# Optimization experiments

Hardware: AMD Instinct MI355X
Metric: run time of the kernel (lower is better)

The kernel has to match this reference:

```python
import jax, jax.numpy as jnp
import numpy as np

B, S, R, Z, NLHS = 1024, 277, 76, 56, 24  # batch, seq_len, n_rules, z_size, n_lhs_symbols


def setup_inputs() -> dict:
    key = jax.random.key(0)
    k1, k2, k3, k4, k5, k6 = jax.random.split(key, 6)
    model_out_x = jax.random.normal(k1, (B, S, R), jnp.float32)
    mu = jax.random.normal(k2, (B, Z), jnp.float32)
    log_var = 0.1 * jax.random.normal(k3, (B, Z), jnp.float32)
    # one-hot targets over rules
    tgt_idx = jax.random.randint(k4, (B, S), 0, R)
    target_x = jax.nn.one_hot(tgt_idx, R, dtype=jnp.float32)
    # binary allowed-transition masks per LHS symbol
    masks = (jax.random.uniform(k5, (NLHS, R)) < 0.3).astype(jnp.float32)
    masks = masks.at[:, 0].set(1.0)  # ensure no all-zero mask row
    ind_to_lhs_ind = jax.random.randint(k6, (R,), 0, NLHS)
    return dict(model_out_x=model_out_x, mu=mu, log_var=log_var,
                target_x=target_x, masks=masks, ind_to_lhs_ind=ind_to_lhs_ind)


def reference(model_out_x, mu, log_var, target_x, masks, ind_to_lhs_ind):
    b = model_out_x.shape[0]
    seq_len = model_out_x.shape[1]
    z_size = mu.shape[1]

    # --- apply_masks: vectorized gather replacing the nested python loops ---
    true_rule = jnp.argmax(target_x, axis=-1)          # [B,S]
    lhs = ind_to_lhs_ind[true_rule]                    # [B,S]
    mask = masks[lhs]                                  # [B,S,R]
    shift_to_tiny = -100.0 + (model_out_x.min() - model_out_x.max())
    x = model_out_x + (1.0 - mask) * shift_to_tiny

    # --- softmax + BCE (torch BCELoss clamps log terms at -100) ---
    p = jax.nn.softmax(x, axis=-1)
    log_p = jnp.maximum(jnp.log(p), -100.0)
    log_1mp = jnp.maximum(jnp.log1p(-p), -100.0)
    bce = -jnp.mean(target_x * log_p + (1.0 - target_x) * log_1mp)
    BCE = seq_len * bce

    # --- moment-matching error on mu ---
    avg_mu = jnp.sum(mu, axis=0) / b                   # [Z]
    var = (mu.T @ mu) / b                              # [Z,Z]
    var_err = var - jnp.eye(z_size, dtype=mu.dtype)
    var_err = jnp.tanh(var_err) * var_err
    mom_err = jnp.sum(avg_mu * avg_mu) / z_size + jnp.sum(var_err) / (z_size * z_size)

    # sample_z=False, module in training mode -> loss = BCE + mom_err
    return BCE + mom_err
```

## Files before the change

### kernel.cpp

```cpp
#include <hip/hip_runtime.h>
#include <math.h>

#define BB    1024
#define SS    277
#define RR    76
#define ZZ    56
#define NLHS  24
#define NROWS (BB*SS)
#define ROWS_PER_BLOCK 256
#define NBCE (NROWS/ROWS_PER_BLOCK)
#define NMOM ZZ
#define NBLK (NBCE + NMOM)
#define F4ROW 19
#define F4BLK (ROWS_PER_BLOCK*F4ROW)
#define BLK_ELEMS (ROWS_PER_BLOCK*RR)
#define TOTAL_ELEMS 21558272.0

static_assert(NROWS % ROWS_PER_BLOCK == 0, "rows divide blocks");

#define LN2F  0.69314718056f
#define NLN2F (-144.26950409f)

__device__ __forceinline__ void gload_lds16(const float4* g, float4* l) {
    auto gp = reinterpret_cast<const __attribute__((address_space(1))) unsigned int*>(
        reinterpret_cast<uintptr_t>(g));
    auto lp = reinterpret_cast<__attribute__((address_space(3))) unsigned int*>(
        reinterpret_cast<uintptr_t>(l));
    __builtin_amdgcn_global_load_lds(gp, lp, 16, 0, 0);
}

__global__ __launch_bounds__(256, 2) void fused_kernel(
    const float* __restrict__ model,
    const float* __restrict__ target,
    const float* __restrict__ masks,
    const int*   __restrict__ ind_to_lhs,
    const float* __restrict__ mu,
    double* __restrict__ partials)
{
    __shared__ float4        sx[F4BLK];
    __shared__ unsigned int  smb[NLHS*4];
    __shared__ int           sm_lhs[RR];
    __shared__ unsigned char sm_idx[ROWS_PER_BLOCK];
    __shared__ float         sm_red[4];
    __shared__ float         sdot[4][64];
    __shared__ float         ssum[4];

    const int tid = threadIdx.x;

    if (blockIdx.x < NMOM) {
        const int j    = blockIdx.x;
        const int w    = tid >> 6;
        const int lane = tid & 63;
        const int i    = (lane < ZZ) ? lane : 0;
        float dot = 0.f, s1 = 0.f;
        const int b0 = 256*w;
        #pragma unroll 4
        for (int b = b0; b < b0 + 256; ++b) {
            const float c = mu[b*ZZ + j];
            const float a = mu[b*ZZ + i];
            dot = fmaf(a, c, dot);
            s1 += c;
        }
        sdot[w][lane] = dot;
        if (lane == 0) ssum[w] = s1;
        __syncthreads();
        if (w == 0) {
            float term = 0.f;
            if (lane < ZZ) {
                const float var = (sdot[0][lane]+sdot[1][lane]+sdot[2][lane]+sdot[3][lane]) * (1.f/BB);
                const float ve  = var - ((lane == j) ? 1.f : 0.f);
                term = tanhf(ve) * ve * (1.f/(ZZ*ZZ));
                if (lane == j) {
                    const float am = (ssum[0]+ssum[1]+ssum[2]+ssum[3]) * (1.f/BB);
                    term = fmaf(am*am, 1.f/ZZ, term);
                }
            }
            #pragma unroll
            for (int off = 32; off; off >>= 1) term += __shfl_xor(term, off, 64);
            if (lane == 0) partials[blockIdx.x] = (double)term;
        }
        return;
    }

    const int bce_blk = blockIdx.x - NMOM;
    const size_t blk_base = (size_t)bce_blk * BLK_ELEMS;

    if (tid < NLHS*4) smb[tid] = 0u;
    sm_idx[tid] = 0;
    __syncthreads();

    float4 t[F4ROW];
    {
        const float4* t4 = (const float4*)(target + blk_base);
        #pragma unroll
        for (int k = 0; k < F4ROW; ++k) t[k] = t4[tid + 256*k];
    }
    {
        const float4* g4 = (const float4*)(model + blk_base);
        #pragma unroll
        for (int k = 0; k < F4ROW; ++k)
            gload_lds16(g4 + tid + 256*k, &sx[tid + 256*k]);
    }

    for (int e = tid; e < NLHS*RR; e += 256) {
        const int lhs = e / RR;
        const int r   = e - lhs*RR;
        if (masks[e] > 0.5f)
            atomicOr(&smb[lhs*4 + (r >> 5)], 1u << (r & 31));
    }
    if (tid < RR) sm_lhs[tid] = ind_to_lhs[tid];

    #pragma unroll
    for (int k = 0; k < F4ROW; ++k) {
        const int v4 = tid + 256*k;
        const float4 tv = t[k];
        int he = -1;
        const int e = v4*4;
        if (tv.x > 0.5f) he = e;
        if (tv.y > 0.5f) he = e+1;
        if (tv.z > 0.5f) he = e+2;
        if (tv.w > 0.5f) he = e+3;
        if (he >= 0) {
            const int row = he / RR;
            sm_idx[row] = (unsigned char)(he - row*RR);
        }
    }
    __syncthreads();

    const int true_r = (int)sm_idx[tid];
    const int lhs    = sm_lhs[true_r];
    const unsigned int mw0 = smb[lhs*4 + 0];
    const unsigned int mw1 = smb[lhs*4 + 1];
    const unsigned int mw2 = smb[lhs*4 + 2];

    const float4* xr = &sx[tid*F4ROW];

    float mx = -1e30f;
    #pragma unroll
    for (int k = 0; k < F4ROW; ++k) {
        const float4 v = xr[k];
        #pragma unroll
        for (int c = 0; c < 4; ++c) {
            const int r = k*4 + c;
            const unsigned int mw = (r < 32) ? mw0 : ((r < 64) ? mw1 : mw2);
            const bool un = (mw >> (r & 31)) & 1u;
            const float xm = un ? (&v.x)[c] : -1e30f;
            mx = fmaxf(mx, xm);
        }
    }

    float s = 0.f;
    #pragma unroll
    for (int k = 0; k < F4ROW; ++k) {
        const float4 v = xr[k];
        #pragma unroll
        for (int c = 0; c < 4; ++c) {
            const int r = k*4 + c;
            const unsigned int mw = (r < 32) ? mw0 : ((r < 64) ? mw1 : mw2);
            const bool un = (mw >> (r & 31)) & 1u;
            const float xm = un ? (&v.x)[c] : -1e30f;
            s += __expf(xm - mx);
        }
    }

    const float inv = 1.f / s;
    float sum_l2 = 0.f;
    float p_true = 0.f;
    #pragma unroll
    for (int k = 0; k < F4ROW; ++k) {
        const float4 v = xr[k];
        #pragma unroll
        for (int c = 0; c < 4; ++c) {
            const int r = k*4 + c;
            const unsigned int mw = (r < 32) ? mw0 : ((r < 64) ? mw1 : mw2);
            const bool un = (mw >> (r & 31)) & 1u;
            const float xm = un ? (&v.x)[c] : -1e30f;
            const float ev = __expf(xm - mx);
            const float p  = ev * inv;
            const float l2 = __log2f(1.f - p);
            sum_l2 += fmaxf(l2, NLN2F);
            if (r == true_r) p_true = p;
        }
    }
    float row_sum = LN2F * sum_l2;
    const float l1c_t = fmaxf(LN2F * __log2f(1.f - p_true), -100.f);
    const float lp_t  = fmaxf(__logf(p_true), -100.f);
    row_sum += lp_t - l1c_t;

    #pragma unroll
    for (int off = 32; off; off >>= 1) row_sum += __shfl_xor(row_sum, off, 64);
    if ((tid & 63) == 0) sm_red[tid >> 6] = row_sum;
    __syncthreads();
    if (tid == 0)
        partials[blockIdx.x] = (double)((sm_red[0] + sm_red[1]) + (sm_red[2] + sm_red[3]));
}

__global__ __launch_bounds__(256) void final_kernel(
    const double* __restrict__ partials, float* __restrict__ out)
{
    __shared__ double sred[4];
    const int tid = threadIdx.x;
    double s = 0.0;
    for (int k = NMOM + tid; k < NBLK; k += 256) s += partials[k];
    double m = (tid < NMOM) ? partials[tid] : 0.0;
    double val = s * (-(double)SS / TOTAL_ELEMS) + m;
    #pragma unroll
    for (int off = 32; off; off >>= 1) val += __shfl_xor(val, off, 64);
    if ((tid & 63) == 0) sred[tid >> 6] = val;
    __syncthreads();
    if (tid == 0) out[0] = (float)((sred[0] + sred[1]) + (sred[2] + sred[3]));
}

extern "C" void kernel_launch(void* const* d_in, const int* in_sizes, int n_in,
                              void* d_out, int out_size, void* d_ws, size_t ws_size,
                              hipStream_t stream) {
    const float* model  = (const float*)d_in[0];
    const float* mu     = (const float*)d_in[1];
    const float* target = (const float*)d_in[3];
    const float* masks  = (const float*)d_in[4];
    const int*   ind    = (const int*)  d_in[5];
    float* out  = (float*)d_out;
    double* acc = (double*)d_ws;

    fused_kernel<<<NBLK, ROWS_PER_BLOCK, 0, stream>>>(model, target, masks, ind, mu, acc);
    final_kernel<<<1, 256, 0, stream>>>(acc, out);
}
```

Baseline: 215.4 us.

## Convert BCE blocks to persistent loop with double-buffered LDS prefetch

The BCE part of the kernel now launches a fixed 256 blocks instead of one block per 256-row group. Each block loops over groups with a stride of 256. While it computes the current group, it fetches the next group's target one-hot indices and issues global-to-LDS loads of the model logits into a second LDS buffer. The goal is to hide global memory latency behind the softmax/BCE math and to cut per-block launch and setup cost. In exchange, LDS use doubles to about 155KB per block, so each CU holds one block of 4 waves instead of two. With 1108 groups the work also ends unevenly: some blocks run 5 iterations and others 4.

```diff
diff --git a/kernel.cpp b/kernel.cpp
--- a/kernel.cpp
+++ b/kernel.cpp
@@ -11,12 +11,13 @@
 #define NBCE (NROWS/ROWS_PER_BLOCK)
 #define NMOM ZZ
 #define NBLK (NBCE + NMOM)
+#define PBLK 256
 #define F4ROW 19
 #define F4BLK (ROWS_PER_BLOCK*F4ROW)
 #define BLK_ELEMS (ROWS_PER_BLOCK*RR)
 #define TOTAL_ELEMS 21558272.0
 
-static_assert(NROWS % ROWS_PER_BLOCK == 0, "rows divide blocks");
+static_assert(NROWS % ROWS_PER_BLOCK == 0, "rows divide groups");
 
 #define LN2F  0.69314718056f
 #define NLN2F (-144.26950409f)
@@ -29,7 +30,7 @@
     __builtin_amdgcn_global_load_lds(gp, lp, 16, 0, 0);
 }
 
-__global__ __launch_bounds__(256, 2) void fused_kernel(
+__global__ __launch_bounds__(256, 1) void fused_kernel(
     const float* __restrict__ model,
     const float* __restrict__ target,
     const float* __restrict__ masks,
@@ -37,11 +38,11 @@
     const float* __restrict__ mu,
     double* __restrict__ partials)
 {
-    __shared__ float4        sx[F4BLK];
+    __shared__ float4        sx[2][F4BLK];
     __shared__ unsigned int  smb[NLHS*4];
     __shared__ int           sm_lhs[RR];
-    __shared__ unsigned char sm_idx[ROWS_PER_BLOCK];
-    __shared__ float         sm_red[4];
+    __shared__ unsigned char sm_idx[2][ROWS_PER_BLOCK];
+    __shared__ float         sm_red[2][4];
     __shared__ float         sdot[4][64];
     __shared__ float         ssum[4];
 
@@ -82,25 +83,12 @@
         return;
     }
 
-    const int bce_blk = blockIdx.x - NMOM;
-    const size_t blk_base = (size_t)bce_blk * BLK_ELEMS;
+    const int bce0 = blockIdx.x - NMOM;
 
     if (tid < NLHS*4) smb[tid] = 0u;
-    sm_idx[tid] = 0;
+    sm_idx[0][tid] = 0;
+    sm_idx[1][tid] = 0;
     __syncthreads();
-
-    float4 t[F4ROW];
-    {
-        const float4* t4 = (const float4*)(target + blk_base);
-        #pragma unroll
-        for (int k = 0; k < F4ROW; ++k) t[k] = t4[tid + 256*k];
-    }
-    {
-        const float4* g4 = (const float4*)(model + blk_base);
-        #pragma unroll
-        for (int k = 0; k < F4ROW; ++k)
-            gload_lds16(g4 + tid + 256*k, &sx[tid + 256*k]);
-    }
 
     for (int e = tid; e < NLHS*RR; e += 256) {
         const int lhs = e / RR;
@@ -110,89 +98,131 @@
     }
     if (tid < RR) sm_lhs[tid] = ind_to_lhs[tid];
 
-    #pragma unroll
-    for (int k = 0; k < F4ROW; ++k) {
-        const int v4 = tid + 256*k;
-        const float4 tv = t[k];
-        int he = -1;
-        const int e = v4*4;
-        if (tv.x > 0.5f) he = e;
-        if (tv.y > 0.5f) he = e+1;
-        if (tv.z > 0.5f) he = e+2;
-        if (tv.w > 0.5f) he = e+3;
-        if (he >= 0) {
-            const int row = he / RR;
-            sm_idx[row] = (unsigned char)(he - row*RR);
+    {
+        const size_t base = (size_t)bce0 * BLK_ELEMS;
+        const float4* g4 = (const float4*)(model + base);
+        #pragma unroll
+        for (int k = 0; k < F4ROW; ++k)
+            gload_lds16(g4 + tid + 256*k, &sx[0][tid + 256*k]);
+        const float4* t4 = (const float4*)(target + base);
+        #pragma unroll
+        for (int k = 0; k < F4ROW; ++k) {
+            const int v4 = tid + 256*k;
+            const float4 tv = t4[v4];
+            int he = -1;
+            const int e = v4*4;
+            if (tv.x > 0.5f) he = e;
+            if (tv.y > 0.5f) he = e+1;
+            if (tv.z > 0.5f) he = e+2;
+            if (tv.w > 0.5f) he = e+3;
+            if (he >= 0) {
+                const int row = he / RR;
+                sm_idx[0][row] = (unsigned char)(he - row*RR);
+            }
         }
     }
     __syncthreads();
 
-    const int true_r = (int)sm_idx[tid];
-    const int lhs    = sm_lhs[true_r];
-    const unsigned int mw0 = smb[lhs*4 + 0];
-    const unsigned int mw1 = smb[lhs*4 + 1];
-    const unsigned int mw2 = smb[lhs*4 + 2];
-
-    const float4* xr = &sx[tid*F4ROW];
-
-    float mx = -1e30f;
-    #pragma unroll
-    for (int k = 0; k < F4ROW; ++k) {
-        const float4 v = xr[k];
-        #pragma unroll
-        for (int c = 0; c < 4; ++c) {
-            const int r = k*4 + c;
-            const unsigned int mw = (r < 32) ? mw0 : ((r < 64) ? mw1 : mw2);
-            const bool un = (mw >> (r & 31)) & 1u;
-            const float xm = un ? (&v.x)[c] : -1e30f;
-            mx = fmaxf(mx, xm);
-        }
-    }
-
-    float s = 0.f;
-    #pragma unroll
-    for (int k = 0; k < F4ROW; ++k) {
-        const float4 v = xr[k];
-        #pragma unroll
-        for (int c = 0; c < 4; ++c) {
-            const int r = k*4 + c;
-            const unsigned int mw = (r < 32) ? mw0 : ((r < 64) ? mw1 : mw2);
-            const bool un = (mw >> (r & 31)) & 1u;
-            const float xm = un ? (&v.x)[c] : -1e30f;
-            s += __expf(xm - mx);
-        }
-    }
-
-    const float inv = 1.f / s;
-    float sum_l2 = 0.f;
-    float p_true = 0.f;
-    #pragma unroll
-    for (int k = 0; k < F4ROW; ++k) {
-        const float4 v = xr[k];
-        #pragma unroll
-        for (int c = 0; c < 4; ++c) {
-            const int r = k*4 + c;
-            const unsigned int mw = (r < 32) ? mw0 : ((r < 64) ? mw1 : mw2);
-            const bool un = (mw >> (r & 31)) & 1u;
-            const float xm = un ? (&v.x)[c] : -1e30f;
-            const float ev = __expf(xm - mx);
-            const float p  = ev * inv;
-            const float l2 = __log2f(1.f - p);
-            sum_l2 += fmaxf(l2, NLN2F);
-            if (r == true_r) p_true = p;
-        }
-    }
-    float row_sum = LN2F * sum_l2;
-    const float l1c_t = fmaxf(LN2F * __log2f(1.f - p_true), -100.f);
-    const float lp_t  = fmaxf(__logf(p_true), -100.f);
-    row_sum += lp_t - l1c_t;
-
-    #pragma unroll
-    for (int off = 32; off; off >>= 1) row_sum += __shfl_xor(row_sum, off, 64);
-    if ((tid & 63) == 0) sm_red[tid >> 6] = row_sum;
-    __syncthreads();
-    if (tid == 0)
-        partials[blockIdx.x] = (double)((sm_red[0] + sm_red[1]) + (sm_red[2] + sm_red[3]));
+    int nb = 0;
+    for (int g = bce0; g < NBCE; g += PBLK) {
+        const int g2 = g + PBLK;
+
+        if (g2 < NBCE) {
+            const size_t base2 = (size_t)g2 * BLK_ELEMS;
+            const float4* t4 = (const float4*)(target + base2);
+            float4 t[F4ROW];
+            #pragma unroll
+            for (int k = 0; k < F4ROW; ++k) t[k] = t4[tid + 256*k];
+            const float4* g4 = (const float4*)(model + base2);
+            #pragma unroll
+            for (int k = 0; k < F4ROW; ++k)
+                gload_lds16(g4 + tid + 256*k, &sx[nb^1][tid + 256*k]);
+            #pragma unroll
+            for (int k = 0; k < F4ROW; ++k) {
+                const int v4 = tid + 256*k;
+                const float4 tv = t[k];
+                int he = -1;
+                const int e = v4*4;
+                if (tv.x > 0.5f) he = e;
+                if (tv.y > 0.5f) he = e+1;
+                if (tv.z > 0.5f) he = e+2;
+                if (tv.w > 0.5f) he = e+3;
+                if (he >= 0) {
+                    const int row = he / RR;
+                    sm_idx[nb^1][row] = (unsigned char)(he - row*RR);
+                }
+            }
+        }
+
+        const int true_r = (int)sm_idx[nb][tid];
+        const int lhs    = sm_lhs[true_r];
+        const unsigned int mw0 = smb[lhs*4 + 0];
+        const unsigned int mw1 = smb[lhs*4 + 1];
+        const unsigned int mw2 = smb[lhs*4 + 2];
+
+        const float4* xr = &sx[nb][tid*F4ROW];
+
+        float mx = -1e30f;
+        #pragma unroll
+        for (int k = 0; k < F4ROW; ++k) {
+            const float4 v = xr[k];
+            #pragma unroll
+            for (int c = 0; c < 4; ++c) {
+                const int r = k*4 + c;
+                const unsigned int mw = (r < 32) ? mw0 : ((r < 64) ? mw1 : mw2);
+                const bool un = (mw >> (r & 31)) & 1u;
+                const float xm = un ? (&v.x)[c] : -1e30f;
+                mx = fmaxf(mx, xm);
+            }
+        }
+
+        float s = 0.f;
+        #pragma unroll
+        for (int k = 0; k < F4ROW; ++k) {
+            const float4 v = xr[k];
+            #pragma unroll
+            for (int c = 0; c < 4; ++c) {
+                const int r = k*4 + c;
+                const unsigned int mw = (r < 32) ? mw0 : ((r < 64) ? mw1 : mw2);
+                const bool un = (mw >> (r & 31)) & 1u;
+                const float xm = un ? (&v.x)[c] : -1e30f;
+                s += __expf(xm - mx);
+            }
+        }
+
+        const float inv = 1.f / s;
+        float sum_l2 = 0.f;
+        float p_true = 0.f;
+        #pragma unroll
+        for (int k = 0; k < F4ROW; ++k) {
+            const float4 v = xr[k];
+            #pragma unroll
+            for (int c = 0; c < 4; ++c) {
+                const int r = k*4 + c;
+                const unsigned int mw = (r < 32) ? mw0 : ((r < 64) ? mw1 : mw2);
+                const bool un = (mw >> (r & 31)) & 1u;
+                const float xm = un ? (&v.x)[c] : -1e30f;
+                const float ev = __expf(xm - mx);
+                const float p  = ev * inv;
+                const float l2 = __log2f(1.f - p);
+                sum_l2 += fmaxf(l2, NLN2F);
+                if (r == true_r) p_true = p;
+            }
+        }
+        float row_sum = LN2F * sum_l2;
+        const float l1c_t = fmaxf(LN2F * __log2f(1.f - p_true), -100.f);
+        const float lp_t  = fmaxf(__logf(p_true), -100.f);
+        row_sum += lp_t - l1c_t;
+
+        #pragma unroll
+        for (int off = 32; off; off >>= 1) row_sum += __shfl_xor(row_sum, off, 64);
+        if ((tid & 63) == 0) sm_red[nb][tid >> 6] = row_sum;
+
+        __syncthreads();
+        if (tid == 0)
+            partials[NMOM + g] = (double)((sm_red[nb][0] + sm_red[nb][1]) + (sm_red[nb][2] + sm_red[nb][3]));
+        nb ^= 1;
+    }
 }
 
 __global__ __launch_bounds__(256) void final_kernel(
@@ -222,6 +252,6 @@
     float* out  = (float*)d_out;
     double* acc = (double*)d_ws;
 
-    fused_kernel<<<NBLK, ROWS_PER_BLOCK, 0, stream>>>(model, target, masks, ind, mu, acc);
+    fused_kernel<<<NMOM + PBLK, ROWS_PER_BLOCK, 0, stream>>>(model, target, masks, ind, mu, acc);
     final_kernel<<<1, 256, 0, stream>>>(acc, out);
 }
```

After: 240.3 us. 11.6% more time.

## Split target argmax scan into a separate prepass kernel before BCE

Applied to the files above, without the earlier changes.

Moves the one-hot target scan and the moment-matching computation into a prepass kernel that writes a per-row true-rule byte index to workspace. The BCE kernel then reads only the model logits and the small index array, which lowers register and load pressure per block. This adds an extra kernel launch and a serialization point between the target pass and the model pass, which removes the overlap of the two streams that the fused kernel had.

```diff
diff --git a/kernel.cpp b/kernel.cpp
--- a/kernel.cpp
+++ b/kernel.cpp
@@ -14,9 +14,11 @@
 #define F4ROW 19
 #define F4BLK (ROWS_PER_BLOCK*F4ROW)
 #define BLK_ELEMS (ROWS_PER_BLOCK*RR)
+#define F4TOTAL (NROWS*F4ROW)
+#define SCAN_BLOCKS 2048
 #define TOTAL_ELEMS 21558272.0
 
-static_assert(NROWS % ROWS_PER_BLOCK == 0, "rows divide blocks");
+static_assert(NROWS % ROWS_PER_BLOCK == 0, "rows divide groups");
 
 #define LN2F  0.69314718056f
 #define NLN2F (-144.26950409f)
@@ -29,21 +31,15 @@
     __builtin_amdgcn_global_load_lds(gp, lp, 16, 0, 0);
 }
 
-__global__ __launch_bounds__(256, 2) void fused_kernel(
-    const float* __restrict__ model,
+
+__global__ __launch_bounds__(256) void prepass_kernel(
     const float* __restrict__ target,
-    const float* __restrict__ masks,
-    const int*   __restrict__ ind_to_lhs,
     const float* __restrict__ mu,
+    unsigned char* __restrict__ idx,
     double* __restrict__ partials)
 {
-    __shared__ float4        sx[F4BLK];
-    __shared__ unsigned int  smb[NLHS*4];
-    __shared__ int           sm_lhs[RR];
-    __shared__ unsigned char sm_idx[ROWS_PER_BLOCK];
-    __shared__ float         sm_red[4];
-    __shared__ float         sdot[4][64];
-    __shared__ float         ssum[4];
+    __shared__ float sdot[4][64];
+    __shared__ float ssum[4];
 
     const int tid = threadIdx.x;
 
@@ -82,25 +78,64 @@
         return;
     }
 
-    const int bce_blk = blockIdx.x - NMOM;
-    const size_t blk_base = (size_t)bce_blk * BLK_ELEMS;
+    const float4* t4 = (const float4*)target;
+    const int STRIDE = SCAN_BLOCKS*256;
+    int v4 = (blockIdx.x - NMOM)*256 + tid;
+    while (v4 < F4TOTAL) {
+        const float4 a = t4[v4];
+        const int v4b = v4 + STRIDE;
+        const bool hb = (v4b < F4TOTAL);
+        float4 b;
+        if (hb) b = t4[v4b];
+
+        {
+            int he = -1;
+            const int e = v4*4;
+            if (a.x > 0.5f) he = e;
+            if (a.y > 0.5f) he = e+1;
+            if (a.z > 0.5f) he = e+2;
+            if (a.w > 0.5f) he = e+3;
+            if (he >= 0) {
+                const int row = he / RR;
+                idx[row] = (unsigned char)(he - row*RR);
+            }
+        }
+        if (hb) {
+            int he = -1;
+            const int e = v4b*4;
+            if (b.x > 0.5f) he = e;
+            if (b.y > 0.5f) he = e+1;
+            if (b.z > 0.5f) he = e+2;
+            if (b.w > 0.5f) he = e+3;
+            if (he >= 0) {
+                const int row = he / RR;
+                idx[row] = (unsigned char)(he - row*RR);
+            }
+        }
+        v4 += 2*STRIDE;
+    }
+}
+
+__global__ __launch_bounds__(256, 2) void bce_kernel(
+    const float* __restrict__ model,
+    const float* __restrict__ masks,
+    const int*   __restrict__ ind_to_lhs,
+    const unsigned char* __restrict__ idx,
+    double* __restrict__ partials)
+{
+    __shared__ float4        sx[F4BLK];
+    __shared__ unsigned int  smb[NLHS*4];
+    __shared__ int           sm_lhs[RR];
+    __shared__ float         sm_red[4];
+
+    const int tid = threadIdx.x;
+    const int g   = blockIdx.x;
+    const size_t blk_base = (size_t)g * BLK_ELEMS;
 
     if (tid < NLHS*4) smb[tid] = 0u;
-    sm_idx[tid] = 0;
-    __syncthreads();
-
-    float4 t[F4ROW];
-    {
-        const float4* t4 = (const float4*)(target + blk_base);
-        #pragma unroll
-        for (int k = 0; k < F4ROW; ++k) t[k] = t4[tid + 256*k];
-    }
-    {
-        const float4* g4 = (const float4*)(model + blk_base);
-        #pragma unroll
-        for (int k = 0; k < F4ROW; ++k)
-            gload_lds16(g4 + tid + 256*k, &sx[tid + 256*k]);
-    }
+    __syncthreads();
+
+    const int true_r = (int)idx[(size_t)g * ROWS_PER_BLOCK + tid];
 
     for (int e = tid; e < NLHS*RR; e += 256) {
         const int lhs = e / RR;
@@ -110,24 +145,14 @@
     }
     if (tid < RR) sm_lhs[tid] = ind_to_lhs[tid];
 
-    #pragma unroll
-    for (int k = 0; k < F4ROW; ++k) {
-        const int v4 = tid + 256*k;
-        const float4 tv = t[k];
-        int he = -1;
-        const int e = v4*4;
-        if (tv.x > 0.5f) he = e;
-        if (tv.y > 0.5f) he = e+1;
-        if (tv.z > 0.5f) he = e+2;
-        if (tv.w > 0.5f) he = e+3;
-        if (he >= 0) {
-            const int row = he / RR;
-            sm_idx[row] = (unsigned char)(he - row*RR);
-        }
-    }
-    __syncthreads();
-
-    const int true_r = (int)sm_idx[tid];
+    {
+        const float4* g4 = (const float4*)(model + blk_base);
+        #pragma unroll
+        for (int k = 0; k < F4ROW; ++k)
+            gload_lds16(g4 + tid + 256*k, &sx[tid + 256*k]);
+    }
+    __syncthreads();
+
     const int lhs    = sm_lhs[true_r];
     const unsigned int mw0 = smb[lhs*4 + 0];
     const unsigned int mw1 = smb[lhs*4 + 1];
@@ -192,7 +217,7 @@
     if ((tid & 63) == 0) sm_red[tid >> 6] = row_sum;
     __syncthreads();
     if (tid == 0)
-        partials[blockIdx.x] = (double)((sm_red[0] + sm_red[1]) + (sm_red[2] + sm_red[3]));
+        partials[NMOM + g] = (double)((sm_red[0] + sm_red[1]) + (sm_red[2] + sm_red[3]));
 }
 
 __global__ __launch_bounds__(256) void final_kernel(
@@ -220,8 +245,11 @@
     const float* masks  = (const float*)d_in[4];
     const int*   ind    = (const int*)  d_in[5];
     float* out  = (float*)d_out;
-    double* acc = (double*)d_ws;
-
-    fused_kernel<<<NBLK, ROWS_PER_BLOCK, 0, stream>>>(model, target, masks, ind, mu, acc);
+
+    double*        acc = (double*)d_ws;
+    unsigned char* idx = (unsigned char*)d_ws + (size_t)NBLK * sizeof(double);
+
+    prepass_kernel<<<NMOM + SCAN_BLOCKS, 256, 0, stream>>>(target, mu, idx, acc);
+    bce_kernel<<<NBCE, 256, 0, stream>>>(model, masks, ind, idx, acc);
     final_kernel<<<1, 256, 0, stream>>>(acc, out);
 }
```

New measurement: 233.6 us. +8.5%, slower.

## Make BCE setup wave-local to remove block barriers before softmax

Applied to the files above, without the earlier changes.

Each wavefront now handles its own 64 rows: it loads its own slice of target and model data and builds a private copy of the mask bitsets and the LHS table, so the block-wide __syncthreads before the softmax phase is removed. A manual s_waitcnt vmcnt(0) replaces the barrier as the guard for the async global-to-LDS loads. Shared memory is merged into a union between the moment and BCE paths. In exchange every wave redundantly reads the masks and runs its own atomics, and LDS use goes up slightly for the per-wave tables.

```diff
diff --git a/kernel.cpp b/kernel.cpp
--- a/kernel.cpp
+++ b/kernel.cpp
@@ -14,9 +14,14 @@
 #define F4ROW 19
 #define F4BLK (ROWS_PER_BLOCK*F4ROW)
 #define BLK_ELEMS (ROWS_PER_BLOCK*RR)
+#define ROWS_PER_WAVE 64
+#define F4WAVE (ROWS_PER_WAVE*F4ROW)
+#define NMASK (NLHS*RR)
+#define NMASK4 (NMASK/4)
 #define TOTAL_ELEMS 21558272.0
 
-static_assert(NROWS % ROWS_PER_BLOCK == 0, "rows divide blocks");
+static_assert(NROWS % ROWS_PER_BLOCK == 0, "rows divide groups");
+static_assert(NMASK4*4 == NMASK, "masks divisible by float4");
 
 #define LN2F  0.69314718056f
 #define NLN2F (-144.26950409f)
@@ -28,6 +33,19 @@
         reinterpret_cast<uintptr_t>(l));
     __builtin_amdgcn_global_load_lds(gp, lp, 16, 0, 0);
 }
+
+struct BceShared {
+    float4        sx[F4BLK];
+    unsigned int  swb[4][NLHS*4];
+    int           swl[4][RR];
+    unsigned char sidx[4][ROWS_PER_WAVE];
+    float         sm_red[4];
+};
+struct MomShared {
+    float sdot[4][64];
+    float ssum[4];
+};
+union SharedU { BceShared b; MomShared m; };
 
 __global__ __launch_bounds__(256, 2) void fused_kernel(
     const float* __restrict__ model,
@@ -37,14 +55,7 @@
     const float* __restrict__ mu,
     double* __restrict__ partials)
 {
-    __shared__ float4        sx[F4BLK];
-    __shared__ unsigned int  smb[NLHS*4];
-    __shared__ int           sm_lhs[RR];
-    __shared__ unsigned char sm_idx[ROWS_PER_BLOCK];
-    __shared__ float         sm_red[4];
-    __shared__ float         sdot[4][64];
-    __shared__ float         ssum[4];
-
+    __shared__ SharedU sh;
     const int tid = threadIdx.x;
 
     if (blockIdx.x < NMOM) {
@@ -61,17 +72,17 @@
             dot = fmaf(a, c, dot);
             s1 += c;
         }
-        sdot[w][lane] = dot;
-        if (lane == 0) ssum[w] = s1;
+        sh.m.sdot[w][lane] = dot;
+        if (lane == 0) sh.m.ssum[w] = s1;
         __syncthreads();
         if (w == 0) {
             float term = 0.f;
             if (lane < ZZ) {
-                const float var = (sdot[0][lane]+sdot[1][lane]+sdot[2][lane]+sdot[3][lane]) * (1.f/BB);
+                const float var = (sh.m.sdot[0][lane]+sh.m.sdot[1][lane]+sh.m.sdot[2][lane]+sh.m.sdot[3][lane]) * (1.f/BB);
                 const float ve  = var - ((lane == j) ? 1.f : 0.f);
                 term = tanhf(ve) * ve * (1.f/(ZZ*ZZ));
                 if (lane == j) {
-                    const float am = (ssum[0]+ssum[1]+ssum[2]+ssum[3]) * (1.f/BB);
+                    const float am = (sh.m.ssum[0]+sh.m.ssum[1]+sh.m.ssum[2]+sh.m.ssum[3]) * (1.f/BB);
                     term = fmaf(am*am, 1.f/ZZ, term);
                 }
             }
@@ -83,36 +94,59 @@
     }
 
     const int bce_blk = blockIdx.x - NMOM;
+    const int w    = tid >> 6;
+    const int lane = tid & 63;
     const size_t blk_base = (size_t)bce_blk * BLK_ELEMS;
 
-    if (tid < NLHS*4) smb[tid] = 0u;
-    sm_idx[tid] = 0;
-    __syncthreads();
+    float4 mv[8];
+    {
+        const float4* m4 = (const float4*)masks;
+        #pragma unroll
+        for (int k = 0; k < 7; ++k) mv[k] = m4[lane + 64*k];
+        mv[7] = (lane + 448 < NMASK4) ? m4[lane + 448] : make_float4(0.f,0.f,0.f,0.f);
+    }
+    const int ivA = ind_to_lhs[lane];
+    const int ivB = (lane < RR-64) ? ind_to_lhs[64 + lane] : 0;
 
     float4 t[F4ROW];
     {
-        const float4* t4 = (const float4*)(target + blk_base);
-        #pragma unroll
-        for (int k = 0; k < F4ROW; ++k) t[k] = t4[tid + 256*k];
-    }
+        const float4* t4 = (const float4*)(target + blk_base) + w*F4WAVE;
+        #pragma unroll
+        for (int k = 0; k < F4ROW; ++k) t[k] = t4[k*64 + lane];
+    }
+
     {
-        const float4* g4 = (const float4*)(model + blk_base);
+        const float4* g4 = (const float4*)(model + blk_base) + w*F4WAVE;
+        float4*       l4 = sh.b.sx + w*F4WAVE;
         #pragma unroll
         for (int k = 0; k < F4ROW; ++k)
-            gload_lds16(g4 + tid + 256*k, &sx[tid + 256*k]);
-    }
-
-    for (int e = tid; e < NLHS*RR; e += 256) {
-        const int lhs = e / RR;
-        const int r   = e - lhs*RR;
-        if (masks[e] > 0.5f)
-            atomicOr(&smb[lhs*4 + (r >> 5)], 1u << (r & 31));
-    }
-    if (tid < RR) sm_lhs[tid] = ind_to_lhs[tid];
-
-    #pragma unroll
-    for (int k = 0; k < F4ROW; ++k) {
-        const int v4 = tid + 256*k;
+            gload_lds16(g4 + k*64 + lane, l4 + k*64 + lane);
+    }
+
+    if (lane < 48) { sh.b.swb[w][lane] = 0u; sh.b.swb[w][lane + 48] = 0u; }
+    #pragma unroll
+    for (int k = 0; k < 8; ++k) {
+        const int q = lane + 64*k;
+        if (q < NMASK4) {
+            const float4 m = mv[k];
+            #pragma unroll
+            for (int c = 0; c < 4; ++c) {
+                if ((&m.x)[c] > 0.5f) {
+                    const int e   = q*4 + c;
+                    const int lhs = e / RR;
+                    const int r   = e - lhs*RR;
+                    atomicOr(&sh.b.swb[w][lhs*4 + (r >> 5)], 1u << (r & 31));
+                }
+            }
+        }
+    }
+    sh.b.swl[w][lane] = ivA;
+    if (lane < RR-64) sh.b.swl[w][64 + lane] = ivB;
+    sh.b.sidx[w][lane] = 0;
+
+    #pragma unroll
+    for (int k = 0; k < F4ROW; ++k) {
+        const int v4 = w*F4WAVE + k*64 + lane;
         const float4 tv = t[k];
         int he = -1;
         const int e = v4*4;
@@ -122,18 +156,20 @@
         if (tv.w > 0.5f) he = e+3;
         if (he >= 0) {
             const int row = he / RR;
-            sm_idx[row] = (unsigned char)(he - row*RR);
-        }
-    }
-    __syncthreads();
-
-    const int true_r = (int)sm_idx[tid];
-    const int lhs    = sm_lhs[true_r];
-    const unsigned int mw0 = smb[lhs*4 + 0];
-    const unsigned int mw1 = smb[lhs*4 + 1];
-    const unsigned int mw2 = smb[lhs*4 + 2];
-
-    const float4* xr = &sx[tid*F4ROW];
+            sh.b.sidx[w][row - w*ROWS_PER_WAVE] = (unsigned char)(he - row*RR);
+        }
+    }
+
+    const int true_r = (int)sh.b.sidx[w][lane];
+    const int lhs    = sh.b.swl[w][true_r];
+    const unsigned int mw0 = sh.b.swb[w][lhs*4 + 0];
+    const unsigned int mw1 = sh.b.swb[w][lhs*4 + 1];
+    const unsigned int mw2 = sh.b.swb[w][lhs*4 + 2];
+
+    asm volatile("s_waitcnt vmcnt(0)" ::: "memory");
+    __builtin_amdgcn_sched_barrier(0);
+
+    const float4* xr = &sh.b.sx[(w*ROWS_PER_WAVE + lane)*F4ROW];
 
     float mx = -1e30f;
     #pragma unroll
@@ -189,10 +225,10 @@
 
     #pragma unroll
     for (int off = 32; off; off >>= 1) row_sum += __shfl_xor(row_sum, off, 64);
-    if ((tid & 63) == 0) sm_red[tid >> 6] = row_sum;
+    if (lane == 0) sh.b.sm_red[w] = row_sum;
     __syncthreads();
     if (tid == 0)
-        partials[blockIdx.x] = (double)((sm_red[0] + sm_red[1]) + (sm_red[2] + sm_red[3]));
+        partials[blockIdx.x] = (double)((sh.b.sm_red[0] + sh.b.sm_red[1]) + (sh.b.sm_red[2] + sh.b.sm_red[3]));
 }
 
 __global__ __launch_bounds__(256) void final_kernel(
```

Result: faster. 203.8 us (-5.4%).
